# Optimization experiments

Hardware: AMD Instinct MI355X
Metric: run time of the kernel (lower is better)

Reference implementation:

```python
import jax, jax.numpy as jnp
import numpy as np

B, S, D = 4, 4096, 2048      # batch, seq, model_dim
E = 128                      # emb_dim (hardcoded in module)
H = 128                      # head_dim
TAU = 0.4                    # self.T
BASE = 3.0                   # self.base (gumbel-sigmoid offset)
LN_EPS = 1e-5


def setup_inputs() -> dict:
    key = jax.random.key(0)
    k_x, k_wr, k_wd, k_g = jax.random.split(key, 4)
    x = jax.random.normal(k_x, (B, S, D), dtype=jnp.float32)
    # torch nn.Linear stores weight as [out_features, in_features]
    W_router = jax.random.normal(k_wr, (E, D), dtype=jnp.float32) / np.sqrt(D)
    W_decoder = jax.random.normal(k_wd, (H, E), dtype=jnp.float32) / np.sqrt(E)
    ln_gamma = jnp.ones((E,), dtype=jnp.float32)
    ln_beta = jnp.zeros((E,), dtype=jnp.float32)
    rnn_state = jnp.zeros((E,), dtype=jnp.float32)  # registered buffer, zeros
    # torch: gumbels = -Exp(1).log()  -> standard Gumbel(0,1) noise
    u = jax.random.uniform(k_g, (B, S, H), dtype=jnp.float32, minval=1e-20, maxval=1.0)
    gumbel_noise = -jnp.log(-jnp.log(u))
    return {
        "x": x, "W_router": W_router, "W_decoder": W_decoder,
        "ln_gamma": ln_gamma, "ln_beta": ln_beta, "rnn_state": rnn_state,
        "gumbel_noise": gumbel_noise, "top_k": 32,
    }


def reference(x, W_router, W_decoder, ln_gamma, ln_beta, rnn_state, gumbel_noise, top_k):
    # router linear (no bias): [B,S,D] @ [D,E] -> [B,S,E]
    out = jnp.einsum("bsd,ed->bse", x, W_router)
    full_emb = rnn_state + out
    # LayerNorm over emb dim (biased variance, as torch LayerNorm)
    mu = full_emb.mean(-1, keepdims=True)
    var = full_emb.var(-1, keepdims=True)
    h = (full_emb - mu) / jnp.sqrt(var + LN_EPS) * ln_gamma + ln_beta
    # decoder linear after exact GELU: [B,S,E] @ [E,H] -> [B,S,H]
    logits = jnp.einsum("bse,he->bsh", jax.nn.gelu(h, approximate=False), W_decoder)
    # gumbel-sigmoid (soft): sigmoid((logits + gumbel + offset)/tau)
    binary_approx = jax.nn.sigmoid((logits + gumbel_noise + BASE) / TAU)
    # hard_sample: straight-through round
    binary = jax.lax.stop_gradient(jnp.round(binary_approx) - binary_approx) + binary_approx
    # top-k mask over head_dim
    _, topk_idx = jax.lax.top_k(binary_approx, top_k)            # [B,S,top_k]
    topk_mask = jax.nn.one_hot(topk_idx, H, dtype=binary_approx.dtype).sum(-2)  # [B,S,H]
    cnt = binary.sum(-1, keepdims=True)
    binary = jnp.where(cnt > top_k, topk_mask, binary)
    # fallback: if a token selects nothing, pick argmax of soft scores
    zero_mask = binary.sum(-1, keepdims=True) == 0
    fallback = jax.nn.one_hot(jnp.argmax(binary_approx, axis=-1), H, dtype=binary_approx.dtype)
    binary = jnp.where(zero_mask, fallback, binary)
    binary = binary.reshape(B, S, -1, H)  # [B,S,1,H]
    return binary, binary_approx
```

## Files before the change

### kernel.cpp

```cpp
#include <hip/hip_runtime.h>
#include <math.h>

#define NTOK   16384
#define DDIM   2048
#define EDIM   128
#define HDIM   128
#define TOKT   64
#define KC     32
#define NCH    (DDIM / KC)

typedef __attribute__((ext_vector_type(8))) _Float16 half8;
typedef __attribute__((ext_vector_type(4))) float    f32x4;

__device__ __forceinline__ int swz(int t, int e) {
  return t * EDIM + ((e & 96) | ((e ^ t) & 31));
}

__global__ __launch_bounds__(256)
void conv_w(const float* __restrict__ Wr,
            _Float16* __restrict__ wh, _Float16* __restrict__ wl) {
  const int idx  = (int)blockIdx.x * 256 + (int)threadIdx.x;
  const int lane = idx & 63;
  const int ks   = (idx >> 6) & 63;
  const int nt   = idx >> 12;
  const int n    = nt * 16 + (lane & 15);
  const int k0   = ks * 32 + (lane >> 4) * 8;
  half8 h, l;
#pragma unroll
  for (int j = 0; j < 8; ++j) {
    const float w = Wr[(size_t)n * DDIM + k0 + j] * 32.0f;
    const _Float16 hh = (_Float16)w;
    h[j] = hh;
    l[j] = (_Float16)((w - (float)hh) * 2048.0f);
  }
  *(half8*)(wh + (size_t)idx * 8) = h;
  *(half8*)(wl + (size_t)idx * 8) = l;
}

__global__ __launch_bounds__(1024)
void fused_router(const float* __restrict__ x,
                  const _Float16* __restrict__ wsh,
                  const _Float16* __restrict__ wsl,
                  const float* __restrict__ Wd,
                  const float* __restrict__ gamma,
                  const float* __restrict__ beta,
                  const float* __restrict__ rnn,
                  const float* __restrict__ gum,
                  float* __restrict__ outb,
                  float* __restrict__ outa) {
  __shared__ char smraw[65536];
  _Float16* const xs = (_Float16*)smraw;
  float* const A  = (float*)smraw;
  float* const G4 = (float*)(smraw + 32768);

  const int tid  = (int)threadIdx.x;
  const int wv   = __builtin_amdgcn_readfirstlane(tid >> 6);
  const int lane = tid & 63;
  const int t0   = (int)blockIdx.x * TOKT;

  const int nt   = wv & 7;
  const int mt0  = (wv >> 3) * 2;
  const int mt1  = mt0 + 1;
  const int quad = lane >> 4;
  const int col  = lane & 15;

  const int offA0 = (mt0 * 64 + lane) * 8;
  const int offA1 = (mt1 * 64 + lane) * 8;
  const int offB  = 8192 + nt * 1024 + lane * 8;

  const bool xstage = tid < 256;
  const int  sx_t   = tid >> 2;
  const int  sx_kq  = tid & 3;
  const float* xg   = x + (size_t)(t0 + sx_t) * DDIM + sx_kq * 8;
  const int  sx_off = ((sx_t >> 4) * 64 + sx_kq * 16 + (sx_t & 15)) * 8;

  const bool wstage = wv >= 8;
  const int  ntw    = wv & 7;
  const _Float16* whg = wsh + (size_t)ntw * 32768 + (size_t)lane * 8;
  const _Float16* wlg = wsl + (size_t)ntw * 32768 + (size_t)lane * 8;
  const int  sw_off = 8192 + ntw * 1024 + lane * 8;

  f32x4 hh0 = {0,0,0,0}, cr0 = {0,0,0,0}, hh1 = {0,0,0,0}, cr1 = {0,0,0,0};

  if (xstage) {
    const float4 a = *(const float4*)xg;
    const float4 bq = *(const float4*)(xg + 4);
    half8 h, l;
#pragma unroll
    for (int m = 0; m < 4; ++m) {
      const float v = (&a.x)[m];
      const _Float16 hv = (_Float16)v;
      h[m] = hv; l[m] = (_Float16)((v - (float)hv) * 2048.0f);
    }
#pragma unroll
    for (int m = 0; m < 4; ++m) {
      const float v = (&bq.x)[m];
      const _Float16 hv = (_Float16)v;
      h[m + 4] = hv; l[m + 4] = (_Float16)((v - (float)hv) * 2048.0f);
    }
    *(half8*)&xs[sx_off] = h;
    *(half8*)&xs[2048 + sx_off] = l;
  }
  if (wstage) {
    const half8 h = *(const half8*)whg;
    const half8 l = *(const half8*)wlg;
    *(half8*)&xs[sw_off] = h;
    *(half8*)&xs[sw_off + 512] = l;
  }

  float4 pxa, pxb; half8 pwh, pwl;
  for (int c = 0; c < NCH; ++c) {
    __syncthreads();
    const int b  = c & 1;
    const int bn = b ^ 1;
    if (c + 1 < NCH) {
      if (xstage) {
        pxa = *(const float4*)(xg + (c + 1) * KC);
        pxb = *(const float4*)(xg + (c + 1) * KC + 4);
      }
      if (wstage) {
        pwh = *(const half8*)(whg + (size_t)(c + 1) * 512);
        pwl = *(const half8*)(wlg + (size_t)(c + 1) * 512);
      }
    }
    const half8 ah0 = *(const half8*)&xs[b * 4096 + offA0];
    const half8 al0 = *(const half8*)&xs[b * 4096 + 2048 + offA0];
    const half8 ah1 = *(const half8*)&xs[b * 4096 + offA1];
    const half8 al1 = *(const half8*)&xs[b * 4096 + 2048 + offA1];
    const half8 bh  = *(const half8*)&xs[b * 8192 + offB];
    const half8 bl  = *(const half8*)&xs[b * 8192 + offB + 512];

    hh0 = __builtin_amdgcn_mfma_f32_16x16x32_f16(ah0, bh, hh0, 0, 0, 0);
    cr0 = __builtin_amdgcn_mfma_f32_16x16x32_f16(ah0, bl, cr0, 0, 0, 0);
    cr0 = __builtin_amdgcn_mfma_f32_16x16x32_f16(al0, bh, cr0, 0, 0, 0);
    hh1 = __builtin_amdgcn_mfma_f32_16x16x32_f16(ah1, bh, hh1, 0, 0, 0);
    cr1 = __builtin_amdgcn_mfma_f32_16x16x32_f16(ah1, bl, cr1, 0, 0, 0);
    cr1 = __builtin_amdgcn_mfma_f32_16x16x32_f16(al1, bh, cr1, 0, 0, 0);

    if (c + 1 < NCH) {
      if (xstage) {
        half8 h, l;
#pragma unroll
        for (int m = 0; m < 4; ++m) {
          const float v = (&pxa.x)[m];
          const _Float16 hv = (_Float16)v;
          h[m] = hv; l[m] = (_Float16)((v - (float)hv) * 2048.0f);
        }
#pragma unroll
        for (int m = 0; m < 4; ++m) {
          const float v = (&pxb.x)[m];
          const _Float16 hv = (_Float16)v;
          h[m + 4] = hv; l[m + 4] = (_Float16)((v - (float)hv) * 2048.0f);
        }
        *(half8*)&xs[bn * 4096 + sx_off] = h;
        *(half8*)&xs[bn * 4096 + 2048 + sx_off] = l;
      }
      if (wstage) {
        *(half8*)&xs[bn * 8192 + sw_off] = pwh;
        *(half8*)&xs[bn * 8192 + sw_off + 512] = pwl;
      }
    }
  }
  __syncthreads();

  {
    const int e  = nt * 16 + col;
    const float rv = rnn[e];
#pragma unroll
    for (int r = 0; r < 4; ++r) {
      A[swz(mt0 * 16 + quad * 4 + r, e)] =
          hh0[r] * (1.0f / 32.0f) + cr0[r] * (1.0f / 65536.0f) + rv;
      A[swz(mt1 * 16 + quad * 4 + r, e)] =
          hh1[r] * (1.0f / 32.0f) + cr1[r] * (1.0f / 65536.0f) + rv;
    }
  }
  __syncthreads();

  const int e0 = wv * 8;
  {
    const float gm0 = gamma[lane], gm1 = gamma[lane + 64];
    const float bt0 = beta[lane],  bt1 = beta[lane + 64];
    for (int tt = wv * 4; tt < wv * 4 + 4; ++tt) {
      const float v0 = A[swz(tt, lane)];
      const float v1 = A[swz(tt, lane + 64)];
      float s = v0 + v1;
#pragma unroll
      for (int m = 32; m; m >>= 1) s += __shfl_xor(s, m);
      const float mu = s * (1.0f / 128.0f);
      const float d0 = v0 - mu, d1 = v1 - mu;
      float q = d0 * d0 + d1 * d1;
#pragma unroll
      for (int m = 32; m; m >>= 1) q += __shfl_xor(q, m);
      const float rstd = 1.0f / sqrtf(q * (1.0f / 128.0f) + 1e-5f);
      const float h0v = d0 * rstd * gm0 + bt0;
      const float h1v = d1 * rstd * gm1 + bt1;
      const float g0 = 0.5f * h0v * (1.0f + erff(h0v * 0.70710678118654752f));
      const float g1 = 0.5f * h1v * (1.0f + erff(h1v * 0.70710678118654752f));
      const int e0a = lane, e1a = lane + 64;
      G4[(tt * 32 + (((e0a >> 2) ^ (tt & 31)))) * 4 + (e0a & 3)] = g0;
      G4[(tt * 32 + (((e1a >> 2) ^ (tt & 31)))) * 4 + (e1a & 3)] = g1;
    }
  }
  __syncthreads();

  {
    float acc2[8];
#pragma unroll
    for (int j = 0; j < 8; ++j) acc2[j] = 0.0f;
    const float4* wd4 = (const float4*)(Wd + (size_t)e0 * EDIM);
#pragma unroll 2
    for (int kg = 0; kg < EDIM / 4; ++kg) {
      const float4 gv = *(const float4*)&G4[(lane * 32 + (kg ^ (lane & 31))) * 4];
#pragma unroll
      for (int j = 0; j < 8; ++j) {
        const float4 w = wd4[(size_t)j * (EDIM / 4) + kg];
        acc2[j] = fmaf(gv.x, w.x,
                  fmaf(gv.y, w.y,
                  fmaf(gv.z, w.z,
                  fmaf(gv.w, w.w, acc2[j]))));
      }
    }
    __syncthreads();
#pragma unroll
    for (int j = 0; j < 8; ++j) A[swz(lane, e0 + j)] = acc2[j];
  }
  __syncthreads();

  for (int tt = wv * 4; tt < wv * 4 + 4; ++tt) {
    const size_t T = (size_t)(t0 + tt);
    const float l0 = A[swz(tt, lane)];
    const float l1 = A[swz(tt, lane + 64)];
    const float gn0 = gum[T * HDIM + lane];
    const float gn1 = gum[T * HDIM + lane + 64];
    const float z0 = (l0 + gn0 + 3.0f) * 2.5f;
    const float z1 = (l1 + gn1 + 3.0f) * 2.5f;
    const float ba0 = 1.0f / (1.0f + expf(-z0));
    const float ba1 = 1.0f / (1.0f + expf(-z1));
    const unsigned ub0 = __float_as_uint(ba0);
    const unsigned ub1 = __float_as_uint(ba1);
    const int r0 = ba0 > 0.5f;
    const int r1 = ba1 > 0.5f;
    const int cnt = __popcll(__ballot(r0)) + __popcll(__ballot(r1));
    float bin0, bin1;
    if (cnt > 32) {
      unsigned v = 0u;
#pragma unroll
      for (int b = 29; b >= 0; --b) {
        const unsigned cand = v | (1u << b);
        const int cc = __popcll(__ballot(ub0 >= cand)) + __popcll(__ballot(ub1 >= cand));
        if (cc >= 32) v = cand;
      }
      const int cgt = __popcll(__ballot(ub0 > v)) + __popcll(__ballot(ub1 > v));
      const int r = 32 - cgt;
      const unsigned long long t0b = __ballot(ub0 == v);
      const unsigned long long t1b = __ballot(ub1 == v);
      const int n0 = __popcll(t0b);
      const unsigned long long mlt = (1ull << lane) - 1ull;
      const int rk0 = __popcll(t0b & mlt);
      const int rk1 = n0 + __popcll(t1b & mlt);
      bin0 = (ub0 > v || (ub0 == v && rk0 < r)) ? 1.0f : 0.0f;
      bin1 = (ub1 > v || (ub1 == v && rk1 < r)) ? 1.0f : 0.0f;
    } else if (cnt == 0) {
      float m = fmaxf(ba0, ba1);
#pragma unroll
      for (int mm = 32; mm; mm >>= 1) m = fmaxf(m, __shfl_xor(m, mm));
      const unsigned long long e0b = __ballot(ba0 == m);
      const unsigned long long e1b = __ballot(ba1 == m);
      const int hstar = e0b ? (__ffsll((unsigned long long)e0b) - 1)
                            : (64 + __ffsll((unsigned long long)e1b) - 1);
      bin0 = (lane == hstar) ? 1.0f : 0.0f;
      bin1 = (lane + 64 == hstar) ? 1.0f : 0.0f;
    } else {
      bin0 = r0 ? 1.0f : 0.0f;
      bin1 = r1 ? 1.0f : 0.0f;
    }
    outb[T * HDIM + lane]      = bin0;
    outb[T * HDIM + lane + 64] = bin1;
    outa[T * HDIM + lane]      = ba0;
    outa[T * HDIM + lane + 64] = ba1;
  }
}

extern "C" void kernel_launch(void* const* d_in, const int* in_sizes, int n_in,
                              void* d_out, int out_size, void* d_ws, size_t ws_size,
                              hipStream_t stream) {
  (void)in_sizes; (void)n_in; (void)ws_size; (void)out_size;
  const float* x   = (const float*)d_in[0];
  const float* Wr  = (const float*)d_in[1];
  const float* Wd  = (const float*)d_in[2];
  const float* gm  = (const float*)d_in[3];
  const float* bt  = (const float*)d_in[4];
  const float* rnn = (const float*)d_in[5];
  const float* gum = (const float*)d_in[6];
  float* outb = (float*)d_out;
  float* outa = outb + (size_t)NTOK * HDIM;

  _Float16* wh = (_Float16*)d_ws;
  _Float16* wl = wh + (size_t)EDIM * DDIM;

  conv_w<<<dim3(128), dim3(256), 0, stream>>>(Wr, wh, wl);
  fused_router<<<dim3(NTOK / TOKT), dim3(1024), 0, stream>>>(
      x, wh, wl, Wd, gm, bt, rnn, gum, outb, outa);
}
```

Baseline: 259.7 us.

## Halve token tile, load router weights straight to registers, shrink blocks

Cuts the token tile from 64 to 32 and the block from 1024 to 512 threads. Each wave now owns one 16-column output tile across both token sub-tiles and loads its router-weight fragments straight from global memory into registers with register prefetch. Only the x tile is staged in LDS, which cuts shared memory to 32KB and allows more resident blocks per CU. The trade-off is that weight fragments are read from global or L2 by twice as many blocks. The decoder stage now has half the lanes computing redundantly.

```diff
diff --git a/kernel.cpp b/kernel.cpp
--- a/kernel.cpp
+++ b/kernel.cpp
@@ -5,11 +5,12 @@
 #define DDIM   2048
 #define EDIM   128
 #define HDIM   128
-#define TOKT   64
+#define TOKT   32
 #define KC     32
 #define NCH    (DDIM / KC)
 
 typedef __attribute__((ext_vector_type(8))) _Float16 half8;
+typedef __attribute__((ext_vector_type(4))) _Float16 half4;
 typedef __attribute__((ext_vector_type(4))) float    f32x4;
 
 __device__ __forceinline__ int swz(int t, int e) {
@@ -37,7 +38,7 @@
   *(half8*)(wl + (size_t)idx * 8) = l;
 }
 
-__global__ __launch_bounds__(1024)
+__global__ __launch_bounds__(512, 4)
 void fused_router(const float* __restrict__ x,
                   const _Float16* __restrict__ wsh,
                   const _Float16* __restrict__ wsl,
@@ -48,87 +49,62 @@
                   const float* __restrict__ gum,
                   float* __restrict__ outb,
                   float* __restrict__ outa) {
-  __shared__ char smraw[65536];
+  __shared__ char smraw[32768];
   _Float16* const xs = (_Float16*)smraw;
   float* const A  = (float*)smraw;
-  float* const G4 = (float*)(smraw + 32768);
+  float* const G4 = (float*)(smraw + 16384);
 
   const int tid  = (int)threadIdx.x;
   const int wv   = __builtin_amdgcn_readfirstlane(tid >> 6);
   const int lane = tid & 63;
   const int t0   = (int)blockIdx.x * TOKT;
 
-  const int nt   = wv & 7;
-  const int mt0  = (wv >> 3) * 2;
-  const int mt1  = mt0 + 1;
+  const int nt   = wv;
   const int quad = lane >> 4;
   const int col  = lane & 15;
 
-  const int offA0 = (mt0 * 64 + lane) * 8;
-  const int offA1 = (mt1 * 64 + lane) * 8;
-  const int offB  = 8192 + nt * 1024 + lane * 8;
+  const int offA0 = col * 32 + quad * 8;
+  const int offA1 = (16 + col) * 32 + quad * 8;
 
   const bool xstage = tid < 256;
-  const int  sx_t   = tid >> 2;
-  const int  sx_kq  = tid & 3;
-  const float* xg   = x + (size_t)(t0 + sx_t) * DDIM + sx_kq * 8;
-  const int  sx_off = ((sx_t >> 4) * 64 + sx_kq * 16 + (sx_t & 15)) * 8;
-
-  const bool wstage = wv >= 8;
-  const int  ntw    = wv & 7;
-  const _Float16* whg = wsh + (size_t)ntw * 32768 + (size_t)lane * 8;
-  const _Float16* wlg = wsl + (size_t)ntw * 32768 + (size_t)lane * 8;
-  const int  sw_off = 8192 + ntw * 1024 + lane * 8;
+  const int  sx_t   = tid >> 3;
+  const int  sx_k   = (tid & 7) * 4;
+  const float* xg   = x + (size_t)(t0 + sx_t) * DDIM + sx_k;
+  const int  sx_off = sx_t * 32 + sx_k;
+
+  const _Float16* whg = wsh + (size_t)nt * 32768 + (size_t)lane * 8;
+  const _Float16* wlg = wsl + (size_t)nt * 32768 + (size_t)lane * 8;
 
   f32x4 hh0 = {0,0,0,0}, cr0 = {0,0,0,0}, hh1 = {0,0,0,0}, cr1 = {0,0,0,0};
 
   if (xstage) {
-    const float4 a = *(const float4*)xg;
-    const float4 bq = *(const float4*)(xg + 4);
-    half8 h, l;
+    const float4 v4 = *(const float4*)xg;
+    half4 h, l;
 #pragma unroll
     for (int m = 0; m < 4; ++m) {
-      const float v = (&a.x)[m];
+      const float v = (&v4.x)[m];
       const _Float16 hv = (_Float16)v;
       h[m] = hv; l[m] = (_Float16)((v - (float)hv) * 2048.0f);
     }
-#pragma unroll
-    for (int m = 0; m < 4; ++m) {
-      const float v = (&bq.x)[m];
-      const _Float16 hv = (_Float16)v;
-      h[m + 4] = hv; l[m + 4] = (_Float16)((v - (float)hv) * 2048.0f);
-    }
-    *(half8*)&xs[sx_off] = h;
-    *(half8*)&xs[2048 + sx_off] = l;
-  }
-  if (wstage) {
-    const half8 h = *(const half8*)whg;
-    const half8 l = *(const half8*)wlg;
-    *(half8*)&xs[sw_off] = h;
-    *(half8*)&xs[sw_off + 512] = l;
-  }
-
-  float4 pxa, pxb; half8 pwh, pwl;
+    *(half4*)&xs[sx_off] = h;
+    *(half4*)&xs[1024 + sx_off] = l;
+  }
+  half8 bh = *(const half8*)whg;
+  half8 bl = *(const half8*)wlg;
+
   for (int c = 0; c < NCH; ++c) {
     __syncthreads();
-    const int b  = c & 1;
-    const int bn = b ^ 1;
+    half8 nbh = bh, nbl = bl; float4 npx;
     if (c + 1 < NCH) {
-      if (xstage) {
-        pxa = *(const float4*)(xg + (c + 1) * KC);
-        pxb = *(const float4*)(xg + (c + 1) * KC + 4);
-      }
-      if (wstage) {
-        pwh = *(const half8*)(whg + (size_t)(c + 1) * 512);
-        pwl = *(const half8*)(wlg + (size_t)(c + 1) * 512);
-      }
-    }
-    const half8 ah0 = *(const half8*)&xs[b * 4096 + offA0];
-    const half8 al0 = *(const half8*)&xs[b * 4096 + 2048 + offA0];
-    const half8 ah1 = *(const half8*)&xs[b * 4096 + offA1];
-    const half8 al1 = *(const half8*)&xs[b * 4096 + 2048 + offA1];
-    const half8 bh  = *(const half8*)&xs[b * 8192 + offB];
-    const half8 bl  = *(const half8*)&xs[b * 8192 + offB + 512];
+      nbh = *(const half8*)(whg + (size_t)(c + 1) * 512);
+      nbl = *(const half8*)(wlg + (size_t)(c + 1) * 512);
+      if (xstage) npx = *(const float4*)(xg + (c + 1) * KC);
+    }
+    const int bo = (c & 1) * 2048;
+    const half8 ah0 = *(const half8*)&xs[bo + offA0];
+    const half8 al0 = *(const half8*)&xs[bo + 1024 + offA0];
+    const half8 ah1 = *(const half8*)&xs[bo + offA1];
+    const half8 al1 = *(const half8*)&xs[bo + 1024 + offA1];
 
     hh0 = __builtin_amdgcn_mfma_f32_16x16x32_f16(ah0, bh, hh0, 0, 0, 0);
     cr0 = __builtin_amdgcn_mfma_f32_16x16x32_f16(ah0, bl, cr0, 0, 0, 0);
@@ -137,29 +113,19 @@
     cr1 = __builtin_amdgcn_mfma_f32_16x16x32_f16(ah1, bl, cr1, 0, 0, 0);
     cr1 = __builtin_amdgcn_mfma_f32_16x16x32_f16(al1, bh, cr1, 0, 0, 0);
 
-    if (c + 1 < NCH) {
-      if (xstage) {
-        half8 h, l;
-#pragma unroll
-        for (int m = 0; m < 4; ++m) {
-          const float v = (&pxa.x)[m];
-          const _Float16 hv = (_Float16)v;
-          h[m] = hv; l[m] = (_Float16)((v - (float)hv) * 2048.0f);
-        }
-#pragma unroll
-        for (int m = 0; m < 4; ++m) {
-          const float v = (&pxb.x)[m];
-          const _Float16 hv = (_Float16)v;
-          h[m + 4] = hv; l[m + 4] = (_Float16)((v - (float)hv) * 2048.0f);
-        }
-        *(half8*)&xs[bn * 4096 + sx_off] = h;
-        *(half8*)&xs[bn * 4096 + 2048 + sx_off] = l;
-      }
-      if (wstage) {
-        *(half8*)&xs[bn * 8192 + sw_off] = pwh;
-        *(half8*)&xs[bn * 8192 + sw_off + 512] = pwl;
-      }
-    }
+    if (c + 1 < NCH && xstage) {
+      const int bn = ((c + 1) & 1) * 2048;
+      half4 h, l;
+#pragma unroll
+      for (int m = 0; m < 4; ++m) {
+        const float v = (&npx.x)[m];
+        const _Float16 hv = (_Float16)v;
+        h[m] = hv; l[m] = (_Float16)((v - (float)hv) * 2048.0f);
+      }
+      *(half4*)&xs[bn + sx_off] = h;
+      *(half4*)&xs[bn + 1024 + sx_off] = l;
+    }
+    bh = nbh; bl = nbl;
   }
   __syncthreads();
 
@@ -168,15 +134,14 @@
     const float rv = rnn[e];
 #pragma unroll
     for (int r = 0; r < 4; ++r) {
-      A[swz(mt0 * 16 + quad * 4 + r, e)] =
+      A[swz(quad * 4 + r, e)] =
           hh0[r] * (1.0f / 32.0f) + cr0[r] * (1.0f / 65536.0f) + rv;
-      A[swz(mt1 * 16 + quad * 4 + r, e)] =
+      A[swz(16 + quad * 4 + r, e)] =
           hh1[r] * (1.0f / 32.0f) + cr1[r] * (1.0f / 65536.0f) + rv;
     }
   }
   __syncthreads();
 
-  const int e0 = wv * 8;
   {
     const float gm0 = gamma[lane], gm1 = gamma[lane + 64];
     const float bt0 = beta[lane],  bt1 = beta[lane + 64];
@@ -204,25 +169,31 @@
   __syncthreads();
 
   {
-    float acc2[8];
-#pragma unroll
-    for (int j = 0; j < 8; ++j) acc2[j] = 0.0f;
-    const float4* wd4 = (const float4*)(Wd + (size_t)e0 * EDIM);
+    const int tok = lane & 31;
+#pragma unroll
+    for (int hb = 0; hb < 2; ++hb) {
+      const int e0h = hb * 64 + wv * 8;
+      float acc2[8];
+#pragma unroll
+      for (int j = 0; j < 8; ++j) acc2[j] = 0.0f;
+      const float4* wd4 = (const float4*)(Wd + (size_t)e0h * EDIM);
 #pragma unroll 2
-    for (int kg = 0; kg < EDIM / 4; ++kg) {
-      const float4 gv = *(const float4*)&G4[(lane * 32 + (kg ^ (lane & 31))) * 4];
-#pragma unroll
-      for (int j = 0; j < 8; ++j) {
-        const float4 w = wd4[(size_t)j * (EDIM / 4) + kg];
-        acc2[j] = fmaf(gv.x, w.x,
-                  fmaf(gv.y, w.y,
-                  fmaf(gv.z, w.z,
-                  fmaf(gv.w, w.w, acc2[j]))));
-      }
-    }
-    __syncthreads();
-#pragma unroll
-    for (int j = 0; j < 8; ++j) A[swz(lane, e0 + j)] = acc2[j];
+      for (int kg = 0; kg < EDIM / 4; ++kg) {
+        const float4 gv = *(const float4*)&G4[(tok * 32 + (kg ^ tok)) * 4];
+#pragma unroll
+        for (int j = 0; j < 8; ++j) {
+          const float4 w = wd4[(size_t)j * (EDIM / 4) + kg];
+          acc2[j] = fmaf(gv.x, w.x,
+                    fmaf(gv.y, w.y,
+                    fmaf(gv.z, w.z,
+                    fmaf(gv.w, w.w, acc2[j]))));
+        }
+      }
+      if (lane < 32) {
+#pragma unroll
+        for (int j = 0; j < 8; ++j) A[swz(tok, e0h + j)] = acc2[j];
+      }
+    }
   }
   __syncthreads();
 
@@ -299,6 +270,6 @@
   _Float16* wl = wh + (size_t)EDIM * DDIM;
 
   conv_w<<<dim3(128), dim3(256), 0, stream>>>(Wr, wh, wl);
-  fused_router<<<dim3(NTOK / TOKT), dim3(1024), 0, stream>>>(
+  fused_router<<<dim3(NTOK / TOKT), dim3(512), 0, stream>>>(
       x, wh, wl, Wd, gm, bt, rnn, gum, outb, outa);
 }
```

Result: slower. 264.9 us (+2.0%).
